# Kernel optimization log

Measured on AMD Instinct MI355X. Metric: run time of the kernel, lower is better.

The kernel has to match this reference:

```python
import jax, jax.numpy as jnp
import numpy as np

B, L, N, H, D, TOPK = 32, 720, 512, 16, 64, 8
TEMP = 1.0


def setup_inputs() -> dict:
    key = jax.random.key(0)
    ks = jax.random.split(key, 18)
    s = lambda k, shp, fan: jax.random.normal(k, shp, jnp.float32) / np.sqrt(fan)
    return {
        'x': jax.random.normal(ks[0], (B, L, N), jnp.float32),
        'var_embed': s(ks[1], (N, H), H),
        'Wq': s(ks[2], (H, H), H), 'bq': jnp.zeros((H,), jnp.float32),
        'Wk': s(ks[3], (H, H), H), 'bk': jnp.zeros((H,), jnp.float32),
        'Wscore': s(ks[4], (N, 1), N), 'bscore': jnp.zeros((1,), jnp.float32),
        'Wc1': s(ks[5], (N, D), N), 'bc1': jnp.zeros((D,), jnp.float32),
        'Wc2': s(ks[6], (D, D), D), 'bc2': jnp.zeros((D,), jnp.float32),
        'Wcn': s(ks[7], (D, N), D), 'bcn': jnp.zeros((N,), jnp.float32),
        'Wg': s(ks[8], (2 * N, N), 2 * N), 'bg': jnp.zeros((N,), jnp.float32),
        'Wf': s(ks[9], (N, N), N), 'bf': jnp.zeros((N,), jnp.float32),
        'gamma': jnp.ones((N,), jnp.float32), 'beta': jnp.zeros((N,), jnp.float32),
    }


def _forward(x, var_embed, Wq, bq, Wk, bk, Wscore, bscore, Wc1, bc1, Wc2, bc2,
             Wcn, bcn, Wg, bg, Wf, bf, gamma, beta):
    # --- SparseVariableRouter (eval mode: no gumbel noise) ---
    Q = var_embed @ Wq + bq          # [N,H]
    K = var_embed @ Wk + bk          # [N,H]
    sim = Q @ K.T                    # [N,N] (identical across batch in torch)
    eye = jnp.eye(N, dtype=bool)
    sim = jnp.where(eye, -1e9, sim)
    topk_vals, topk_idx = jax.lax.top_k(sim, TOPK)      # [N,k]
    w = jax.nn.softmax(topk_vals / TEMP, axis=-1)        # [N,k]
    x_perm = jnp.transpose(x, (0, 2, 1))                 # [B,N,L]
    neighbors = x_perm[:, topk_idx, :]                   # [B,N,k,L] gather
    ring_out = jnp.einsum('bnkl,nk->bln', neighbors, w)  # [B,L,N]
    # --- center path ---
    attn = jax.nn.softmax(x @ Wscore + bscore, axis=1)   # [B,L,1] softmax over L
    center_raw = jnp.sum(x * attn, axis=1)               # [B,N]
    c = jax.nn.gelu(center_raw @ Wc1 + bc1, approximate=False)
    c = jax.nn.gelu(c @ Wc2 + bc2, approximate=False)
    center = c @ Wcn + bcn                               # [B,N]
    center_b = jnp.broadcast_to(center[:, None, :], (x.shape[0], x.shape[1], N))
    # --- gated fusion + residual LN ---
    gate = jax.nn.sigmoid(jnp.concatenate([ring_out, center_b], axis=-1) @ Wg + bg)
    fused = gate * ring_out + (1.0 - gate) * center_b
    fused = fused @ Wf + bf
    h = fused + x
    mu = jnp.mean(h, axis=-1, keepdims=True)
    var = jnp.var(h, axis=-1, keepdims=True)
    return (h - mu) * jax.lax.rsqrt(var + 1e-5) * gamma + beta


def reference(x, var_embed, Wq, bq, Wk, bk, Wscore, bscore, Wc1, bc1, Wc2, bc2,
              Wcn, bcn, Wg, bg, Wf, bf, gamma, beta):
    return _forward(x, var_embed, Wq, bq, Wk, bk, Wscore, bscore, Wc1, bc1,
                    Wc2, bc2, Wcn, bcn, Wg, bg, Wf, bf, gamma, beta)
```

## Files before the change

### kernel.cpp

```cpp
#include <hip/hip_runtime.h>
#include <hip/hip_bf16.h>
#include <math.h>

#define B_ 32
#define L_ 720
#define N_ 512
#define H_ 16
#define D_ 64
#define TOPK_ 8
#define M_ (B_ * L_)
#define RPB 8
#define CRCH 16
#define CRL (L_ / CRCH)

typedef __bf16 bf16x8 __attribute__((ext_vector_type(8)));
typedef float f32x16 __attribute__((ext_vector_type(16)));

__device__ __forceinline__ void async_cp16(const __hip_bfloat16* g, __hip_bfloat16* l) {
    __builtin_amdgcn_global_load_lds(
        (const __attribute__((address_space(1))) void*)g,
        (__attribute__((address_space(3))) void*)l, 16, 0, 0);
}

__device__ __forceinline__ bf16x8 frag_ld(const __hip_bfloat16* base, int row, int j0) {
    return *(const bf16x8*)(base + row * 64 + (((j0) ^ (row & 7)) << 3));
}

__global__ __launch_bounds__(512) void qk_kernel(
    const float* __restrict__ ve,
    const float* __restrict__ Wq, const float* __restrict__ bq,
    const float* __restrict__ Wk, const float* __restrict__ bk,
    float* __restrict__ Qm, float* __restrict__ Km)
{
    const int g = blockIdx.x * 512 + threadIdx.x;
    const int j = g >> 4, h = g & 15;
    const float* vr = ve + j * H_;
    float q = bq[h], k = bk[h];
    #pragma unroll
    for (int m = 0; m < H_; ++m) {
        const float v = vr[m];
        q += v * Wq[m * H_ + h];
        k += v * Wk[m * H_ + h];
    }
    Qm[g] = q;
    Km[g] = k;
}

__global__ __launch_bounds__(64) void topk_kernel(
    const float* __restrict__ Qm, const float* __restrict__ Km,
    float* __restrict__ w_out, int* __restrict__ idx_out)
{
    const int n = blockIdx.x;
    const int lane = threadIdx.x;

    float4 q0, q1, q2, q3;
    {
        const float4* qr = (const float4*)(Qm + n * H_);
        q0 = qr[0]; q1 = qr[1]; q2 = qr[2]; q3 = qr[3];
    }

    float sv[8]; int si[8];
    #pragma unroll
    for (int c = 0; c < 8; ++c) {
        const int j = c * 64 + lane;
        const float4* kr = (const float4*)(Km + j * H_);
        float4 k0 = kr[0], k1 = kr[1], k2 = kr[2], k3 = kr[3];
        float s = q0.x * k0.x + q0.y * k0.y + q0.z * k0.z + q0.w * k0.w
                + q1.x * k1.x + q1.y * k1.y + q1.z * k1.z + q1.w * k1.w
                + q2.x * k2.x + q2.y * k2.y + q2.z * k2.z + q2.w * k2.w
                + q3.x * k3.x + q3.y * k3.y + q3.z * k3.z + q3.w * k3.w;
        sv[c] = (j == n) ? -1e9f : s;
        si[c] = j;
    }

    float keepv[TOPK_]; int keepi[TOPK_];
    #pragma unroll
    for (int k = 0; k < TOPK_; ++k) {
        float bv = sv[0]; int bi = si[0]; int bslot = 0;
        #pragma unroll
        for (int c = 1; c < 8; ++c)
            if (sv[c] > bv || (sv[c] == bv && si[c] < bi)) { bv = sv[c]; bi = si[c]; bslot = c; }
        float v = bv; int i = bi;
        #pragma unroll
        for (int off = 32; off > 0; off >>= 1) {
            float v2 = __shfl_xor(v, off);
            int   i2 = __shfl_xor(i, off);
            if (v2 > v || (v2 == v && i2 < i)) { v = v2; i = i2; }
        }
        keepv[k] = v; keepi[k] = i;
        if (i == bi) sv[bslot] = -INFINITY;
    }

    if (lane == 0) {
        float vmax = keepv[0];
        float ev[TOPK_], esum = 0.f;
        #pragma unroll
        for (int k = 0; k < TOPK_; k++) { ev[k] = expf(keepv[k] - vmax); esum += ev[k]; }
        float inv = 1.f / esum;
        #pragma unroll
        for (int k = 0; k < TOPK_; k++) {
            w_out[n * TOPK_ + k] = ev[k] * inv;
            idx_out[n * TOPK_ + k] = keepi[k];
        }
    }
}

__global__ __launch_bounds__(512) void ring_kernel(
    const float* __restrict__ x, const float* __restrict__ w,
    const int* __restrict__ idx,
    const float* __restrict__ Wscore, const float* __restrict__ bscore,
    __hip_bfloat16* __restrict__ ring, float* __restrict__ s)
{
    __shared__ float xs[RPB][N_];
    __shared__ float wsh[N_ * TOPK_];
    __shared__ int   ish[N_ * TOPK_];
    const int t = threadIdx.x;
    const int row0 = blockIdx.x * RPB;

    for (int i = t; i < N_ * TOPK_; i += 512) { wsh[i] = w[i]; ish[i] = idx[i]; }
    {
        const float4* xg = (const float4*)(x + (size_t)row0 * N_);
        float4* xsf = (float4*)&xs[0][0];
        xsf[t] = xg[t];
        xsf[t + 512] = xg[t + 512];
    }
    __syncthreads();

    {
        const int wv = t >> 6, lane = t & 63;
        float sa = 0.f;
        #pragma unroll
        for (int i = 0; i < 8; ++i) sa += xs[wv][lane + i * 64] * Wscore[lane + i * 64];
        for (int off = 32; off > 0; off >>= 1) sa += __shfl_down(sa, off);
        if (lane == 0) s[row0 + wv] = sa + bscore[0];
    }

    float wr[TOPK_]; int ir[TOPK_];
    #pragma unroll
    for (int k = 0; k < TOPK_; ++k) { wr[k] = wsh[t * TOPK_ + k]; ir[k] = ish[t * TOPK_ + k]; }
    #pragma unroll
    for (int r = 0; r < RPB; ++r) {
        float acc = 0.f;
        #pragma unroll
        for (int k = 0; k < TOPK_; ++k) acc += wr[k] * xs[r][ir[k]];
        ring[(size_t)(row0 + r) * N_ + t] = __float2bfloat16(acc);
    }
}

__global__ __launch_bounds__(256) void attn_softmax_kernel(float* __restrict__ s)
{
    const int b = blockIdx.x;
    const int t = threadIdx.x;
    float* row = s + (size_t)b * L_;

    __shared__ float sm[4];
    __shared__ float sm2[4];

    float lmax = -1e30f;
    for (int l = t; l < L_; l += 256) lmax = fmaxf(lmax, row[l]);
    for (int off = 32; off > 0; off >>= 1) lmax = fmaxf(lmax, __shfl_down(lmax, off));
    if ((t & 63) == 0) sm[t >> 6] = lmax;
    __syncthreads();
    float gmax = fmaxf(fmaxf(sm[0], sm[1]), fmaxf(sm[2], sm[3]));

    float lsum = 0.f;
    for (int l = t; l < L_; l += 256) {
        float e = expf(row[l] - gmax);
        row[l] = e;
        lsum += e;
    }
    for (int off = 32; off > 0; off >>= 1) lsum += __shfl_down(lsum, off);
    if ((t & 63) == 0) sm2[t >> 6] = lsum;
    __syncthreads();
    float inv = 1.f / (sm2[0] + sm2[1] + sm2[2] + sm2[3]);
    for (int l = t; l < L_; l += 256) row[l] *= inv;
}

__global__ __launch_bounds__(512) void center_raw_kernel(
    const float* __restrict__ x, const float* __restrict__ attn,
    float* __restrict__ craw_p)
{
    const int b = blockIdx.x >> 4;
    const int c = blockIdx.x & 15;
    const int n = threadIdx.x;
    __shared__ float ash[CRL];
    const int l0 = c * CRL;
    if (n < CRL) ash[n] = attn[b * L_ + l0 + n];
    __syncthreads();
    const float* xb = x + ((size_t)b * L_ + l0) * N_;
    float acc = 0.f;
    #pragma unroll 3
    for (int l = 0; l < CRL; l++) acc += ash[l] * xb[(size_t)l * N_ + n];
    craw_p[(size_t)(b * CRCH + c) * N_ + n] = acc;
}

__device__ __forceinline__ float gelu_exact(float v) {
    return 0.5f * v * (1.0f + erff(v * 0.70710678118654752440f));
}

__global__ __launch_bounds__(512) void center_mlp_kernel(
    const float* __restrict__ craw_p,
    const float* __restrict__ Wc1, const float* __restrict__ bc1,
    const float* __restrict__ Wc2, const float* __restrict__ bc2,
    const float* __restrict__ Wcn, const float* __restrict__ bcn,
    float* __restrict__ center)
{
    const int b = blockIdx.x;
    const int t = threadIdx.x;
    const int col = t & 63;
    const int seg = t >> 6;
    __shared__ float cr[N_];
    __shared__ float psum[8][D_];
    __shared__ float h1[D_];
    __shared__ float h2[D_];

    {
        float acc = 0.f;
        #pragma unroll
        for (int c = 0; c < CRCH; ++c) acc += craw_p[(size_t)(b * CRCH + c) * N_ + t];
        cr[t] = acc;
    }
    __syncthreads();
    {
        float p = 0.f;
        #pragma unroll 8
        for (int m = seg * 64; m < seg * 64 + 64; ++m) p += cr[m] * Wc1[m * D_ + col];
        psum[seg][col] = p;
    }
    __syncthreads();
    if (t < D_) {
        float acc = bc1[t];
        #pragma unroll
        for (int s2 = 0; s2 < 8; ++s2) acc += psum[s2][t];
        h1[t] = gelu_exact(acc);
    }
    __syncthreads();
    if (t < D_) {
        float acc = bc2[t];
        #pragma unroll 8
        for (int j = 0; j < D_; j++) acc += h1[j] * Wc2[j * D_ + t];
        h2[t] = gelu_exact(acc);
    }
    __syncthreads();
    {
        float acc = bcn[t];
        #pragma unroll 8
        for (int j = 0; j < D_; j++) acc += h2[j] * Wcn[j * N_ + t];
        center[b * N_ + t] = acc;
    }
}

__global__ __launch_bounds__(512) void cg_kernel(
    const float* __restrict__ center, const float* __restrict__ Wg,
    const float* __restrict__ bg, float* __restrict__ cg)
{
    const int nc = blockIdx.x;
    const int b  = blockIdx.y;
    const int t  = threadIdx.x;
    const int col = nc * 64 + (t & 63);
    const int seg = t >> 6;
    __shared__ float cs[N_];
    __shared__ float psum[8][64];

    cs[t] = center[b * N_ + t];
    __syncthreads();
    {
        float p = 0.f;
        const float* wp = Wg + (size_t)(N_ + seg * 64) * N_ + col;
        #pragma unroll 8
        for (int m = 0; m < 64; ++m) { p += cs[seg * 64 + m] * wp[0]; wp += N_; }
        psum[seg][t & 63] = p;
    }
    __syncthreads();
    if (t < 64) {
        float acc = bg[nc * 64 + t];
        #pragma unroll
        for (int s2 = 0; s2 < 8; ++s2) acc += psum[s2][t];
        cg[b * N_ + nc * 64 + t] = acc;
    }
}

__global__ __launch_bounds__(256) void convert_kernel(
    const float* __restrict__ Wg, const float* __restrict__ Wf,
    __hip_bfloat16* __restrict__ WgT, __hip_bfloat16* __restrict__ WfT)
{
    const int n = blockIdx.x & 511;
    const bool isf = blockIdx.x >= 512;
    const float* src = isf ? Wf : Wg;
    __hip_bfloat16* dst = isf ? WfT : WgT;
    for (int k = threadIdx.x; k < N_; k += 256)
        dst[n * N_ + k] = __float2bfloat16(src[(size_t)k * N_ + n]);
}

#define GEMM_BODY(EPILOGUE)                                                    \
    __shared__ __hip_bfloat16 Ash[128 * 64];                                   \
    __shared__ __hip_bfloat16 Bsh[128 * 64];                                   \
    const int tid  = threadIdx.x;                                              \
    const int lane = tid & 63;                                                 \
    const int wv   = tid >> 6;                                                 \
    const int m32  = lane & 31;                                                \
    const int half = lane >> 5;                                                \
    const int wr   = wv >> 1;                                                  \
    const int wc   = wv & 1;                                                   \
    const int row0 = blockIdx.x * 128;                                         \
    const int n0   = blockIdx.y * 128;                                         \
    const int swz  = (lane & 7) ^ (lane >> 3);                                 \
    const int rln  = lane >> 3;                                                \
    f32x16 acc[2][2];                                                          \
    _Pragma("unroll") for (int i = 0; i < 2; i++)                              \
        _Pragma("unroll") for (int j = 0; j < 2; j++)                          \
            _Pragma("unroll") for (int e = 0; e < 16; e++) acc[i][j][e] = 0.f; \
    for (int step = 0; step < 8; ++step) {                                     \
        const int k0 = step * 64;                                              \
        const __hip_bfloat16* Ab = A  + (size_t)row0 * N_ + k0 + swz * 8;      \
        const __hip_bfloat16* Bb = BT + (size_t)n0   * N_ + k0 + swz * 8;      \
        __syncthreads();                                                       \
        _Pragma("unroll") for (int j = 0; j < 4; ++j) {                        \
            const int r = j * 32 + wv * 8 + rln;                               \
            const int lb = (j * 256 + wv * 64) * 8;                            \
            async_cp16(Ab + (size_t)r * N_, Ash + lb);                         \
            async_cp16(Bb + (size_t)r * N_, Bsh + lb);                         \
        }                                                                      \
        __syncthreads();                                                       \
        _Pragma("unroll") for (int ks = 0; ks < 4; ++ks) {                     \
            const int j0 = ks * 2 + half;                                      \
            bf16x8 a0 = frag_ld(Ash, wr * 64      + m32, j0);                  \
            bf16x8 a1 = frag_ld(Ash, wr * 64 + 32 + m32, j0);                  \
            bf16x8 b0 = frag_ld(Bsh, wc * 64      + m32, j0);                  \
            bf16x8 b1 = frag_ld(Bsh, wc * 64 + 32 + m32, j0);                  \
            acc[0][0] = __builtin_amdgcn_mfma_f32_32x32x16_bf16(a0, b0, acc[0][0], 0, 0, 0); \
            acc[0][1] = __builtin_amdgcn_mfma_f32_32x32x16_bf16(a0, b1, acc[0][1], 0, 0, 0); \
            acc[1][0] = __builtin_amdgcn_mfma_f32_32x32x16_bf16(a1, b0, acc[1][0], 0, 0, 0); \
            acc[1][1] = __builtin_amdgcn_mfma_f32_32x32x16_bf16(a1, b1, acc[1][1], 0, 0, 0); \
        }                                                                      \
    }                                                                          \
    _Pragma("unroll") for (int mi = 0; mi < 2; ++mi)                           \
        _Pragma("unroll") for (int ni = 0; ni < 2; ++ni)                       \
            _Pragma("unroll") for (int reg = 0; reg < 16; ++reg) {             \
                const int rg  = row0 + wr * 64 + mi * 32 +                     \
                                (reg & 3) + 8 * (reg >> 2) + 4 * half;         \
                const int col = n0 + wc * 64 + ni * 32 + m32;                  \
                const float aval = acc[mi][ni][reg];                           \
                EPILOGUE                                                       \
            }

__global__ __launch_bounds__(256) void gemm_gate_kernel(
    const __hip_bfloat16* __restrict__ A,
    const __hip_bfloat16* __restrict__ BT,
    const float* __restrict__ cg,
    const float* __restrict__ center,
    __hip_bfloat16* __restrict__ fused)
{
    GEMM_BODY({
        const int b = rg / L_;
        const float logit = aval + cg[b * N_ + col];
        const float g = 1.f / (1.f + expf(-logit));
        const float rv = __bfloat162float(A[(size_t)rg * N_ + col]);
        const float f = g * rv + (1.f - g) * center[b * N_ + col];
        fused[(size_t)rg * N_ + col] = __float2bfloat16(f);
    })
}

__global__ __launch_bounds__(256) void gemm_out_kernel(
    const __hip_bfloat16* __restrict__ A,
    const __hip_bfloat16* __restrict__ BT,
    const float* __restrict__ x,
    const float* __restrict__ bfv,
    float* __restrict__ out)
{
    GEMM_BODY({
        out[(size_t)rg * N_ + col] = aval + bfv[col] + x[(size_t)rg * N_ + col];
    })
}

__global__ __launch_bounds__(512) void ln_kernel(
    float* __restrict__ out,
    const float* __restrict__ gamma, const float* __restrict__ beta)
{
    const int tid = threadIdx.x;
    const int r = tid >> 7;
    const int c = tid & 127;
    const int row = blockIdx.x * 4 + r;
    const int wid = tid >> 6;
    __shared__ float ls[8], lq[8];

    float4 v = ((const float4*)(out + (size_t)row * N_))[c];
    float sum = v.x + v.y + v.z + v.w;
    float sq  = v.x * v.x + v.y * v.y + v.z * v.z + v.w * v.w;
    for (int off = 32; off > 0; off >>= 1) {
        sum += __shfl_down(sum, off);
        sq  += __shfl_down(sq,  off);
    }
    if ((tid & 63) == 0) { ls[wid] = sum; lq[wid] = sq; }
    __syncthreads();
    const float S  = ls[2 * r] + ls[2 * r + 1];
    const float Q2 = lq[2 * r] + lq[2 * r + 1];
    const float mu  = S * (1.0f / N_);
    const float var = Q2 * (1.0f / N_) - mu * mu;
    const float inv = 1.0f / sqrtf(var + 1e-5f);
    const float4 g4 = ((const float4*)gamma)[c];
    const float4 b4 = ((const float4*)beta)[c];
    float4 o;
    o.x = (v.x - mu) * inv * g4.x + b4.x;
    o.y = (v.y - mu) * inv * g4.y + b4.y;
    o.z = (v.z - mu) * inv * g4.z + b4.z;
    o.w = (v.w - mu) * inv * g4.w + b4.w;
    ((float4*)(out + (size_t)row * N_))[c] = o;
}

extern "C" void kernel_launch(void* const* d_in, const int* in_sizes, int n_in,
                              void* d_out, int out_size, void* d_ws, size_t ws_size,
                              hipStream_t stream) {
    const float* x       = (const float*)d_in[0];
    const float* ve      = (const float*)d_in[1];
    const float* Wq      = (const float*)d_in[2];
    const float* bq      = (const float*)d_in[3];
    const float* Wk      = (const float*)d_in[4];
    const float* bk      = (const float*)d_in[5];
    const float* Wscore  = (const float*)d_in[6];
    const float* bscore  = (const float*)d_in[7];
    const float* Wc1     = (const float*)d_in[8];
    const float* bc1     = (const float*)d_in[9];
    const float* Wc2     = (const float*)d_in[10];
    const float* bc2     = (const float*)d_in[11];
    const float* Wcn     = (const float*)d_in[12];
    const float* bcn     = (const float*)d_in[13];
    const float* Wg      = (const float*)d_in[14];
    const float* bg      = (const float*)d_in[15];
    const float* Wf      = (const float*)d_in[16];
    const float* bf      = (const float*)d_in[17];
    const float* gamma   = (const float*)d_in[18];
    const float* beta    = (const float*)d_in[19];
    float* out = (float*)d_out;

    char* p = (char*)d_ws;
    float* ws_w    = (float*)p; p += N_ * TOPK_ * sizeof(float);
    int*   ws_idx  = (int*)p;   p += N_ * TOPK_ * sizeof(int);
    float* ws_s    = (float*)p; p += B_ * L_ * sizeof(float);
    float* ws_crp  = (float*)p; p += B_ * CRCH * N_ * sizeof(float);
    float* ws_cent = (float*)p; p += B_ * N_ * sizeof(float);
    float* ws_cg   = (float*)p; p += B_ * N_ * sizeof(float);
    float* ws_Q    = (float*)p; p += N_ * H_ * sizeof(float);
    float* ws_K    = (float*)p; p += N_ * H_ * sizeof(float);
    __hip_bfloat16* ws_ring  = (__hip_bfloat16*)p; p += (size_t)M_ * N_ * sizeof(__hip_bfloat16);
    __hip_bfloat16* ws_fused = (__hip_bfloat16*)p; p += (size_t)M_ * N_ * sizeof(__hip_bfloat16);
    __hip_bfloat16* ws_WgT   = (__hip_bfloat16*)p; p += (size_t)N_ * N_ * sizeof(__hip_bfloat16);
    __hip_bfloat16* ws_WfT   = (__hip_bfloat16*)p; p += (size_t)N_ * N_ * sizeof(__hip_bfloat16);

    convert_kernel<<<1024, 256, 0, stream>>>(Wg, Wf, ws_WgT, ws_WfT);
    qk_kernel<<<16, 512, 0, stream>>>(ve, Wq, bq, Wk, bk, ws_Q, ws_K);
    topk_kernel<<<N_, 64, 0, stream>>>(ws_Q, ws_K, ws_w, ws_idx);
    ring_kernel<<<M_ / RPB, 512, 0, stream>>>(x, ws_w, ws_idx, Wscore, bscore,
                                              ws_ring, ws_s);
    attn_softmax_kernel<<<B_, 256, 0, stream>>>(ws_s);
    center_raw_kernel<<<B_ * CRCH, 512, 0, stream>>>(x, ws_s, ws_crp);
    center_mlp_kernel<<<B_, 512, 0, stream>>>(ws_crp, Wc1, bc1, Wc2, bc2,
                                              Wcn, bcn, ws_cent);
    cg_kernel<<<dim3(8, B_), 512, 0, stream>>>(ws_cent, Wg, bg, ws_cg);
    dim3 ggrid(M_ / 128, N_ / 128);
    gemm_gate_kernel<<<ggrid, 256, 0, stream>>>(ws_ring, ws_WgT, ws_cg,
                                                ws_cent, ws_fused);
    gemm_out_kernel<<<ggrid, 256, 0, stream>>>(ws_fused, ws_WfT, x, bf, out);
    ln_kernel<<<M_ / 4, 512, 0, stream>>>(out, gamma, beta);
}
```

Measured before the change: 265.1 us.

## Double-buffer GEMM LDS tiles with async prefetch of next K-step

Splits the shared A/B tiles into two buffers and issues the async global-to-LDS loads for the next K-step before computing on the current one. Explicit vmcnt waits and barriers replace the two __syncthreads per step, so global load latency can overlap with the MFMA work. This doubles LDS use per block (64KB), which may reduce occupancy. It also relies on hand-counted vmcnt values being correct.

```diff
diff --git a/kernel.cpp b/kernel.cpp
--- a/kernel.cpp
+++ b/kernel.cpp
@@ -292,9 +292,17 @@
         dst[n * N_ + k] = __float2bfloat16(src[(size_t)k * N_ + n]);
 }
 
+#define GEMM_STAGE(dstA, dstB, k0)                                             \
+    _Pragma("unroll") for (int j = 0; j < 4; ++j) {                            \
+        const int r = j * 32 + wv * 8 + rln;                                   \
+        const int lb = (j * 256 + wv * 64) * 8;                                \
+        async_cp16(Abase + (size_t)r * N_ + (k0), (dstA) + lb);                \
+        async_cp16(Bbase + (size_t)r * N_ + (k0), (dstB) + lb);                \
+    }
+
 #define GEMM_BODY(EPILOGUE)                                                    \
-    __shared__ __hip_bfloat16 Ash[128 * 64];                                   \
-    __shared__ __hip_bfloat16 Bsh[128 * 64];                                   \
+    __shared__ __hip_bfloat16 Ash[2][128 * 64];                                \
+    __shared__ __hip_bfloat16 Bsh[2][128 * 64];                                \
     const int tid  = threadIdx.x;                                              \
     const int lane = tid & 63;                                                 \
     const int wv   = tid >> 6;                                                 \
@@ -306,32 +314,35 @@
     const int n0   = blockIdx.y * 128;                                         \
     const int swz  = (lane & 7) ^ (lane >> 3);                                 \
     const int rln  = lane >> 3;                                                \
+    const __hip_bfloat16* Abase = A  + (size_t)row0 * N_ + swz * 8;            \
+    const __hip_bfloat16* Bbase = BT + (size_t)n0   * N_ + swz * 8;            \
     f32x16 acc[2][2];                                                          \
     _Pragma("unroll") for (int i = 0; i < 2; i++)                              \
         _Pragma("unroll") for (int j = 0; j < 2; j++)                          \
             _Pragma("unroll") for (int e = 0; e < 16; e++) acc[i][j][e] = 0.f; \
-    for (int step = 0; step < 8; ++step) {                                     \
-        const int k0 = step * 64;                                              \
-        const __hip_bfloat16* Ab = A  + (size_t)row0 * N_ + k0 + swz * 8;      \
-        const __hip_bfloat16* Bb = BT + (size_t)n0   * N_ + k0 + swz * 8;      \
-        __syncthreads();                                                       \
-        _Pragma("unroll") for (int j = 0; j < 4; ++j) {                        \
-            const int r = j * 32 + wv * 8 + rln;                               \
-            const int lb = (j * 256 + wv * 64) * 8;                            \
-            async_cp16(Ab + (size_t)r * N_, Ash + lb);                         \
-            async_cp16(Bb + (size_t)r * N_, Bsh + lb);                         \
-        }                                                                      \
-        __syncthreads();                                                       \
+    GEMM_STAGE(Ash[0], Bsh[0], 0)                                              \
+    _Pragma("unroll") for (int step = 0; step < 8; ++step) {                   \
+        const int cur = step & 1;                                              \
+        if (step < 7) { GEMM_STAGE(Ash[cur ^ 1], Bsh[cur ^ 1], (step + 1) * 64) } \
+        if (step < 7) asm volatile("s_waitcnt vmcnt(8)" ::: "memory");         \
+        else          asm volatile("s_waitcnt vmcnt(0)" ::: "memory");         \
+        __builtin_amdgcn_s_barrier();                                          \
+        asm volatile("" ::: "memory");                                         \
         _Pragma("unroll") for (int ks = 0; ks < 4; ++ks) {                     \
             const int j0 = ks * 2 + half;                                      \
-            bf16x8 a0 = frag_ld(Ash, wr * 64      + m32, j0);                  \
-            bf16x8 a1 = frag_ld(Ash, wr * 64 + 32 + m32, j0);                  \
-            bf16x8 b0 = frag_ld(Bsh, wc * 64      + m32, j0);                  \
-            bf16x8 b1 = frag_ld(Bsh, wc * 64 + 32 + m32, j0);                  \
+            bf16x8 a0 = frag_ld(Ash[cur], wr * 64      + m32, j0);             \
+            bf16x8 a1 = frag_ld(Ash[cur], wr * 64 + 32 + m32, j0);             \
+            bf16x8 b0 = frag_ld(Bsh[cur], wc * 64      + m32, j0);             \
+            bf16x8 b1 = frag_ld(Bsh[cur], wc * 64 + 32 + m32, j0);             \
             acc[0][0] = __builtin_amdgcn_mfma_f32_32x32x16_bf16(a0, b0, acc[0][0], 0, 0, 0); \
             acc[0][1] = __builtin_amdgcn_mfma_f32_32x32x16_bf16(a0, b1, acc[0][1], 0, 0, 0); \
             acc[1][0] = __builtin_amdgcn_mfma_f32_32x32x16_bf16(a1, b0, acc[1][0], 0, 0, 0); \
             acc[1][1] = __builtin_amdgcn_mfma_f32_32x32x16_bf16(a1, b1, acc[1][1], 0, 0, 0); \
+        }                                                                      \
+        if (step < 7) {                                                        \
+            asm volatile("s_waitcnt lgkmcnt(0)" ::: "memory");                 \
+            __builtin_amdgcn_s_barrier();                                      \
+            asm volatile("" ::: "memory");                                     \
         }                                                                      \
     }                                                                          \
     _Pragma("unroll") for (int mi = 0; mi < 2; ++mi)                           \
```

Measured after the change: 309.5 us. 1.17x slower.
